# Performance work log

Measured on AMD Instinct MI355X. Metric: run time of the kernel, lower is better.

## Reference

```python
import jax, jax.numpy as jnp
import numpy as np

C = 256; HEADS = 8; LEVELS = 4; POINTS = 4; D = C // HEADS
SPATIAL = np.array([[96, 96], [48, 48], [24, 24], [12, 12]], dtype=np.int32)  # (H, W) per level
AREAS = SPATIAL[:, 0] * SPATIAL[:, 1]
HW = int(AREAS.sum())  # 12240
LSI = np.concatenate([[0], np.cumsum(AREAS)[:-1]]).astype(np.int32)
N = 1; Q = HW


def setup_inputs() -> dict:
    key = jax.random.key(0)
    ks = jax.random.split(key, 12)
    s = 0.02
    return {
        "query": jax.random.normal(ks[0], (N, Q, C), jnp.float32),
        "reference_points": jax.random.uniform(ks[1], (N, Q, LEVELS, 2), jnp.float32),
        "input_flatten": jax.random.normal(ks[2], (N, HW, C), jnp.float32),
        "input_spatial_shapes": jnp.asarray(SPATIAL),
        "input_level_start_index": jnp.asarray(LSI),
        "W_off": jax.random.normal(ks[3], (C, HEADS * LEVELS * POINTS * 2), jnp.float32) * s,
        "b_off": jax.random.normal(ks[4], (HEADS * LEVELS * POINTS * 2,), jnp.float32) * s,
        "W_attn": jax.random.normal(ks[5], (C, HEADS * LEVELS * POINTS), jnp.float32) * s,
        "b_attn": jax.random.normal(ks[6], (HEADS * LEVELS * POINTS,), jnp.float32) * s,
        "W_val": jax.random.normal(ks[7], (C, C), jnp.float32) * (1.0 / np.sqrt(C)),
        "b_val": jax.random.normal(ks[8], (C,), jnp.float32) * s,
        "W_out": jax.random.normal(ks[9], (C, C), jnp.float32) * (1.0 / np.sqrt(C)),
        "b_out": jax.random.normal(ks[10], (C,), jnp.float32) * s,
    }


def _ms_deform_attn(query, reference_points, input_flatten, sp, lsi,
                    W_off, b_off, W_attn, b_attn, W_val, b_val, W_out, b_out):
    n, q, c = query.shape
    hw = input_flatten.shape[1]
    # value projection -> [N, Hd, HW, D]
    value = (input_flatten @ W_val + b_val).reshape(n, hw, HEADS, D).transpose(0, 2, 1, 3)
    # sampling offsets [N,Q,Hd,L,P,2]
    off = (query @ W_off + b_off).reshape(n, q, HEADS, LEVELS, POINTS, 2)
    # attention weights softmaxed over L*P (done inside the fused CUDA kernel)
    attn = jax.nn.softmax((query @ W_attn + b_attn).reshape(n, q, HEADS, LEVELS * POINTS), axis=-1)
    attn = attn.reshape(n, q, HEADS, LEVELS, POINTS)
    # normalized sampling locations (reference_points last dim == 2 branch)
    norm = jnp.stack([sp[:, 1], sp[:, 0]], -1).astype(query.dtype)  # (W, H) per level
    loc = reference_points[:, :, None, :, None, :] + off / norm[None, None, None, :, None, :]
    Hl = sp[:, 0][None, None, None, :, None]
    Wl = sp[:, 1][None, None, None, :, None]
    start = lsi[None, None, None, :, None]
    # grid_sample-style (align_corners=False) pixel coordinates
    x = loc[..., 0] * Wl - 0.5
    y = loc[..., 1] * Hl - 0.5
    x0 = jnp.floor(x); y0 = jnp.floor(y)
    lx = x - x0; ly = y - y0
    x0i = x0.astype(jnp.int32); y0i = y0.astype(jnp.int32)

    def gather(yi, xi):
        valid = (xi >= 0) & (xi < Wl) & (yi >= 0) & (yi < Hl)
        idx = jnp.where(valid, start + yi * Wl + xi, 0)  # [N,Q,Hd,L,P]
        idx_t = idx.transpose(0, 2, 1, 3, 4).reshape(n, HEADS, q * LEVELS * POINTS, 1)
        g = jnp.take_along_axis(value, idx_t, axis=2)  # [N,Hd,Q*L*P,D]
        g = g.reshape(n, HEADS, q, LEVELS, POINTS, D)
        return g * valid.transpose(0, 2, 1, 3, 4)[..., None]

    def w(a):
        return a.transpose(0, 2, 1, 3, 4)[..., None]  # [N,Hd,Q,L,P,1]

    sampled = (gather(y0i, x0i) * w((1 - ly) * (1 - lx))
               + gather(y0i, x0i + 1) * w((1 - ly) * lx)
               + gather(y0i + 1, x0i) * w(ly * (1 - lx))
               + gather(y0i + 1, x0i + 1) * w(ly * lx))  # [N,Hd,Q,L,P,D]
    out = jnp.einsum('nhqlpd,nqhlp->nqhd', sampled, attn).reshape(n, q, c)
    return out @ W_out + b_out


def reference(query, reference_points, input_flatten, input_spatial_shapes, input_level_start_index,
              W_off, b_off, W_attn, b_attn, W_val, b_val, W_out, b_out):
    return _ms_deform_attn(query, reference_points, input_flatten,
                           input_spatial_shapes, input_level_start_index,
                           W_off, b_off, W_attn, b_attn, W_val, b_val, W_out, b_out)
```

## Files before the change

kernel.cpp:

```cpp
#include <hip/hip_runtime.h>

#define QTOT 12240
#define KD   256

typedef float f32x4 __attribute__((ext_vector_type(4)));
typedef short s16x8 __attribute__((ext_vector_type(8)));
typedef short s16x4 __attribute__((ext_vector_type(4)));
typedef unsigned short ushort_t;

__device__ __forceinline__ unsigned short f2b(float x) {
    union { float f; unsigned u; } c; c.f = x;
    unsigned r = c.u + 0x7fffu + ((c.u >> 16) & 1u);
    return (unsigned short)(r >> 16);
}
__device__ __forceinline__ int swz(int row, int kb) { return row * 512 + (kb ^ ((row & 7) << 4)); }

__global__ __launch_bounds__(256) void prep(
    const float* __restrict__ W_val, const float* __restrict__ W_off,
    const float* __restrict__ W_attn, const float* __restrict__ W_out,
    const float* __restrict__ b_off, const float* __restrict__ b_attn,
    ushort_t* __restrict__ WvT, ushort_t* __restrict__ WcT,
    ushort_t* __restrict__ WoT, float* __restrict__ bcomb)
{
    int id = blockIdx.x * 256 + threadIdx.x;
    if (id < 65536) { int n = id >> 8, k = id & 255; WvT[id] = f2b(W_val[k * 256 + n]); }
    else if (id < 163840) {
        int t = id - 65536; int n = t >> 8, k = t & 255;
        float v = (n < 256) ? W_off[k * 256 + n] : W_attn[k * 128 + (n - 256)];
        WcT[t] = f2b(v);
    } else if (id < 229376) {
        int t = id - 163840; int n = t >> 8, k = t & 255;
        WoT[t] = f2b(W_out[k * 256 + n]);
    } else if (id < 229760) {
        int t = id - 229376; bcomb[t] = (t < 256) ? b_off[t] : b_attn[t - 256];
    }
}

__global__ __launch_bounds__(256) void gemm1(
    const float* __restrict__ inflat, const float* __restrict__ query,
    const ushort_t* __restrict__ WvT, const ushort_t* __restrict__ WcT,
    const float* __restrict__ b_val, const float* __restrict__ bcomb,
    ushort_t* __restrict__ projb, ushort_t* __restrict__ offb,
    float* __restrict__ logitf)
{
    __shared__ char As[16384];
    const int b = blockIdx.x;
    const bool isval = b < 383;
    const int bm = (isval ? b : b - 383) * 32;
    const float* A = isval ? inflat : query;
    const ushort_t* WT = isval ? WvT : WcT;
    const int nc = isval ? 4 : 6;

    const int tid = threadIdx.x, lane = tid & 63, wave = tid >> 6;
    const int lr = lane & 15, g8 = (lane >> 4) * 8;

    {
        const float4* srcb = (const float4*)(A + (size_t)bm * KD);
        const int rem_rows = QTOT - bm;
#pragma unroll
        for (int j = 0; j < 8; ++j) {
            const int f4i = j * 256 + tid;
            const int row = f4i >> 6;
            const int colb = (f4i & 63) * 8;
            float4 f = make_float4(0.f, 0.f, 0.f, 0.f);
            if (row < rem_rows) f = srcb[f4i];
            s16x4 v;
            v[0] = f2b(f.x); v[1] = f2b(f.y); v[2] = f2b(f.z); v[3] = f2b(f.w);
            *(s16x4*)(As + swz(row, colb)) = v;
        }
    }
    __syncthreads();

    const int rg = (lane >> 4) * 4;

    for (int c = 0; c < nc; ++c) {
        const int col = c * 64 + wave * 16 + lr;
        s16x8 bfr[8];
        {
            const ushort_t* bp = WT + (size_t)col * KD + g8;
#pragma unroll
            for (int kc = 0; kc < 8; ++kc) bfr[kc] = *(const s16x8*)(bp + kc * 32);
        }
        f32x4 acc[2];
        acc[0] = (f32x4)0.f; acc[1] = (f32x4)0.f;
#pragma unroll
        for (int kc = 0; kc < 8; ++kc) {
            const int kb = (kc * 32 + g8) * 2;
            s16x8 a0 = *(const s16x8*)(As + swz(lr,      kb));
            s16x8 a1 = *(const s16x8*)(As + swz(16 + lr, kb));
            acc[0] = __builtin_amdgcn_mfma_f32_16x16x32_bf16(a0, bfr[kc], acc[0], 0, 0, 0);
            acc[1] = __builtin_amdgcn_mfma_f32_16x16x32_bf16(a1, bfr[kc], acc[1], 0, 0, 0);
        }
        const float bb = isval ? b_val[col] : bcomb[col];
#pragma unroll
        for (int mf = 0; mf < 2; ++mf)
#pragma unroll
            for (int rr = 0; rr < 4; ++rr) {
                const int row = bm + mf * 16 + rg + rr;
                if (row >= QTOT) continue;
                const float v = acc[mf][rr] + bb;
                if (isval)          projb[(size_t)row * 256 + col] = f2b(v);
                else if (col < 256) offb [(size_t)row * 256 + col] = f2b(v);
                else                logitf[(size_t)row * 128 + col - 256] = v;
            }
    }
}

__global__ __launch_bounds__(256) void sample5(
    const float* __restrict__ rp, const ushort_t* __restrict__ offb,
    const float* __restrict__ logitf, const ushort_t* __restrict__ projb,
    const int* __restrict__ sp, const int* __restrict__ lsi,
    ushort_t* __restrict__ outpre)
{
    const int q0 = blockIdx.x * 4;
    const int tid = threadIdx.x;

    __shared__ int   s_idx[512][4];
    __shared__ float s_w[512][4];

#pragma unroll
    for (int rep = 0; rep < 2; ++rep) {
        const int task = rep * 256 + tid;
        const int ql = task >> 7, t = task & 127;
        const int l = (t >> 2) & 3;
        const int q = q0 + ql;

        float logit = logitf[(size_t)q * 128 + t];
        float mx = logit;
#pragma unroll
        for (int d = 1; d < 16; d <<= 1) mx = fmaxf(mx, __shfl_xor(mx, d));
        float e = __expf(logit - mx);
        float s = e;
#pragma unroll
        for (int d = 1; d < 16; d <<= 1) s += __shfl_xor(s, d);
        const float aw = e / s;

        const unsigned opk = *(const unsigned*)&offb[(size_t)q * 256 + t * 2];
        const float ox = __uint_as_float(opk << 16);
        const float oy = __uint_as_float(opk & 0xffff0000u);

        const int Hl = sp[l * 2], Wl = sp[l * 2 + 1], st = lsi[l];
        const float rx = rp[((size_t)q * 4 + l) * 2 + 0];
        const float ry = rp[((size_t)q * 4 + l) * 2 + 1];

        const float x = rx * (float)Wl + ox - 0.5f;
        const float y = ry * (float)Hl + oy - 0.5f;
        const float xf = floorf(x), yf = floorf(y);
        const int x0 = (int)xf, y0 = (int)yf;
        const float lx = x - xf, ly = y - yf;

        const bool vx0 = (x0 >= 0) && (x0 < Wl);
        const bool vx1 = (x0 + 1 >= 0) && (x0 + 1 < Wl);
        const bool vy0 = (y0 >= 0) && (y0 < Hl);
        const bool vy1 = (y0 + 1 >= 0) && (y0 + 1 < Hl);

        s_w[task][0] = (vx0 && vy0) ? aw * (1.f - ly) * (1.f - lx) : 0.f;
        s_w[task][1] = (vx1 && vy0) ? aw * (1.f - ly) * lx         : 0.f;
        s_w[task][2] = (vx0 && vy1) ? aw * ly * (1.f - lx)         : 0.f;
        s_w[task][3] = (vx1 && vy1) ? aw * ly * lx                 : 0.f;
        s_idx[task][0] = (vx0 && vy0) ? (st + y0 * Wl + x0) * 512           : 0;
        s_idx[task][1] = (vx1 && vy0) ? (st + y0 * Wl + x0 + 1) * 512       : 0;
        s_idx[task][2] = (vx0 && vy1) ? (st + (y0 + 1) * Wl + x0) * 512     : 0;
        s_idx[task][3] = (vx1 && vy1) ? (st + (y0 + 1) * Wl + x0 + 1) * 512 : 0;
    }
    __syncthreads();

    const int t = tid & 127, qlA = tid >> 7;
    const int h = t >> 4, pq = (t >> 2) & 3, c8 = t & 3;
    const char* basec = (const char*)projb + (h * 32 + c8 * 8) * 2;

    float aA[8] = {0,0,0,0,0,0,0,0};
    float aB[8] = {0,0,0,0,0,0,0,0};
#pragma unroll
    for (int l = 0; l < 4; ++l) {
        const int slotA = (qlA << 7)       + h * 16 + l * 4 + pq;
        const int slotB = ((qlA + 2) << 7) + h * 16 + l * 4 + pq;
        const int4   iA = *(const int4*)s_idx[slotA];
        const float4 wA = *(const float4*)s_w[slotA];
        const int4   iB = *(const int4*)s_idx[slotB];
        const float4 wB = *(const float4*)s_w[slotB];
#pragma unroll
        for (int c = 0; c < 4; ++c) {
            const int   idA = (c == 0) ? iA.x : (c == 1) ? iA.y : (c == 2) ? iA.z : iA.w;
            const float wwA = (c == 0) ? wA.x : (c == 1) ? wA.y : (c == 2) ? wA.z : wA.w;
            const uint4 v = *(const uint4*)(basec + idA);
            aA[0] += wwA * __uint_as_float(v.x << 16);
            aA[1] += wwA * __uint_as_float(v.x & 0xffff0000u);
            aA[2] += wwA * __uint_as_float(v.y << 16);
            aA[3] += wwA * __uint_as_float(v.y & 0xffff0000u);
            aA[4] += wwA * __uint_as_float(v.z << 16);
            aA[5] += wwA * __uint_as_float(v.z & 0xffff0000u);
            aA[6] += wwA * __uint_as_float(v.w << 16);
            aA[7] += wwA * __uint_as_float(v.w & 0xffff0000u);
        }
#pragma unroll
        for (int c = 0; c < 4; ++c) {
            const int   idB = (c == 0) ? iB.x : (c == 1) ? iB.y : (c == 2) ? iB.z : iB.w;
            const float wwB = (c == 0) ? wB.x : (c == 1) ? wB.y : (c == 2) ? wB.z : wB.w;
            const uint4 v = *(const uint4*)(basec + idB);
            aB[0] += wwB * __uint_as_float(v.x << 16);
            aB[1] += wwB * __uint_as_float(v.x & 0xffff0000u);
            aB[2] += wwB * __uint_as_float(v.y << 16);
            aB[3] += wwB * __uint_as_float(v.y & 0xffff0000u);
            aB[4] += wwB * __uint_as_float(v.z << 16);
            aB[5] += wwB * __uint_as_float(v.z & 0xffff0000u);
            aB[6] += wwB * __uint_as_float(v.w << 16);
            aB[7] += wwB * __uint_as_float(v.w & 0xffff0000u);
        }
    }
#pragma unroll
    for (int i = 0; i < 8; ++i) {
        aA[i] += __shfl_xor(aA[i], 4);  aA[i] += __shfl_xor(aA[i], 8);
        aB[i] += __shfl_xor(aB[i], 4);  aB[i] += __shfl_xor(aB[i], 8);
    }
    if (pq == 0) {
        const int colo = h * 32 + c8 * 8;
        uint4 o;
        o.x = (unsigned)f2b(aA[0]) | ((unsigned)f2b(aA[1]) << 16);
        o.y = (unsigned)f2b(aA[2]) | ((unsigned)f2b(aA[3]) << 16);
        o.z = (unsigned)f2b(aA[4]) | ((unsigned)f2b(aA[5]) << 16);
        o.w = (unsigned)f2b(aA[6]) | ((unsigned)f2b(aA[7]) << 16);
        *(uint4*)&outpre[(size_t)(q0 + qlA) * 256 + colo] = o;
        o.x = (unsigned)f2b(aB[0]) | ((unsigned)f2b(aB[1]) << 16);
        o.y = (unsigned)f2b(aB[2]) | ((unsigned)f2b(aB[3]) << 16);
        o.z = (unsigned)f2b(aB[4]) | ((unsigned)f2b(aB[5]) << 16);
        o.w = (unsigned)f2b(aB[6]) | ((unsigned)f2b(aB[7]) << 16);
        *(uint4*)&outpre[(size_t)(q0 + qlA + 2) * 256 + colo] = o;
    }
}

__global__ __launch_bounds__(256) void gemm_o(
    const ushort_t* __restrict__ Ab, const ushort_t* __restrict__ WoT,
    const float* __restrict__ b_out, float* __restrict__ out)
{
    const int bm = blockIdx.x * 32;
    const int tid = threadIdx.x, lane = tid & 63, wave = tid >> 6;
    const int lr = lane & 15, g8 = (lane >> 4) * 8;
    const int rg = (lane >> 4) * 4;

    const ushort_t* ap0;
    const ushort_t* ap1;
    {
        int r0 = bm + lr;      if (r0 >= QTOT) r0 = QTOT - 1;
        int r1 = bm + 16 + lr; if (r1 >= QTOT) r1 = QTOT - 1;
        ap0 = Ab + (size_t)r0 * KD + g8;
        ap1 = Ab + (size_t)r1 * KD + g8;
    }

#pragma unroll
    for (int c = 0; c < 4; ++c) {
        const int col = c * 64 + wave * 16 + lr;
        s16x8 bfr[8];
        {
            const ushort_t* bp = WoT + (size_t)col * KD + g8;
#pragma unroll
            for (int kc = 0; kc < 8; ++kc) bfr[kc] = *(const s16x8*)(bp + kc * 32);
        }
        f32x4 acc[2];
        acc[0] = (f32x4)0.f; acc[1] = (f32x4)0.f;
#pragma unroll
        for (int kc = 0; kc < 8; ++kc) {
            s16x8 a0 = *(const s16x8*)(ap0 + kc * 32);
            s16x8 a1 = *(const s16x8*)(ap1 + kc * 32);
            acc[0] = __builtin_amdgcn_mfma_f32_16x16x32_bf16(a0, bfr[kc], acc[0], 0, 0, 0);
            acc[1] = __builtin_amdgcn_mfma_f32_16x16x32_bf16(a1, bfr[kc], acc[1], 0, 0, 0);
        }
        const float bb = b_out[col];
#pragma unroll
        for (int mf = 0; mf < 2; ++mf)
#pragma unroll
            for (int rr = 0; rr < 4; ++rr) {
                const int row = bm + mf * 16 + rg + rr;
                if (row < QTOT) out[(size_t)row * 256 + col] = acc[mf][rr] + bb;
            }
    }
}

extern "C" void kernel_launch(void* const* d_in, const int* in_sizes, int n_in,
                              void* d_out, int out_size, void* d_ws, size_t ws_size,
                              hipStream_t stream) {
    const float* query  = (const float*)d_in[0];
    const float* rp     = (const float*)d_in[1];
    const float* inflat = (const float*)d_in[2];
    const int*   sp     = (const int*)d_in[3];
    const int*   lsi    = (const int*)d_in[4];
    const float* W_off  = (const float*)d_in[5];
    const float* b_off  = (const float*)d_in[6];
    const float* W_attn = (const float*)d_in[7];
    const float* b_attn = (const float*)d_in[8];
    const float* W_val  = (const float*)d_in[9];
    const float* b_val  = (const float*)d_in[10];
    const float* W_out  = (const float*)d_in[11];
    const float* b_out  = (const float*)d_in[12];
    float* out = (float*)d_out;

    char* ws = (char*)d_ws;
    ushort_t* projb  = (ushort_t*)ws; ws += (size_t)QTOT * 256 * 2;
    ushort_t* offb   = (ushort_t*)ws; ws += (size_t)QTOT * 256 * 2;
    float*    logitf = (float*)ws;    ws += (size_t)QTOT * 128 * 4;
    ushort_t* outpre = (ushort_t*)ws; ws += (size_t)QTOT * 256 * 2;
    ushort_t* WvT    = (ushort_t*)ws; ws += 65536 * 2;
    ushort_t* WcT    = (ushort_t*)ws; ws += 98304 * 2;
    ushort_t* WoT    = (ushort_t*)ws; ws += 65536 * 2;
    float*    bcomb  = (float*)ws;    ws += 384 * 4;

    prep<<<dim3(898), dim3(256), 0, stream>>>(W_val, W_off, W_attn, W_out, b_off, b_attn,
                                              WvT, WcT, WoT, bcomb);

    gemm1<<<dim3(766), dim3(256), 0, stream>>>(inflat, query, WvT, WcT, b_val, bcomb,
                                               projb, offb, logitf);

    sample5<<<dim3(3060), dim3(256), 0, stream>>>(rp, offb, logitf, projb, sp, lsi, outpre);

    gemm_o<<<dim3(383), dim3(256), 0, stream>>>(outpre, WoT, b_out, out);
}
```

Before: 69.72 us.

## Tile-transpose weight prep, double-buffer B fragments, store logits as bf16, retile output GEMM

Weight prep now transposes each 32x32 tile through shared memory with coalesced float4 reads and vector stores, replacing strided scalar gathers. Both GEMM kernels now prefetch the next column chunk's B fragments while running MFMA on the current chunk. Attention logits are stored as bf16 instead of fp32, halving that intermediate's traffic at some precision cost in the softmax inputs. The output GEMM uses 16-row tiles, giving twice as many blocks, and keeps its A fragments in registers.

```diff
diff --git a/kernel.cpp b/kernel.cpp
--- a/kernel.cpp
+++ b/kernel.cpp
@@ -13,26 +13,92 @@
     unsigned r = c.u + 0x7fffu + ((c.u >> 16) & 1u);
     return (unsigned short)(r >> 16);
 }
+__device__ __forceinline__ float b2f(unsigned short u) {
+    return __uint_as_float((unsigned)u << 16);
+}
 __device__ __forceinline__ int swz(int row, int kb) { return row * 512 + (kb ^ ((row & 7) << 4)); }
 
-__global__ __launch_bounds__(256) void prep(
+__global__ __launch_bounds__(256) void prep2(
     const float* __restrict__ W_val, const float* __restrict__ W_off,
     const float* __restrict__ W_attn, const float* __restrict__ W_out,
     const float* __restrict__ b_off, const float* __restrict__ b_attn,
     ushort_t* __restrict__ WvT, ushort_t* __restrict__ WcT,
     ushort_t* __restrict__ WoT, float* __restrict__ bcomb)
 {
-    int id = blockIdx.x * 256 + threadIdx.x;
-    if (id < 65536) { int n = id >> 8, k = id & 255; WvT[id] = f2b(W_val[k * 256 + n]); }
-    else if (id < 163840) {
-        int t = id - 65536; int n = t >> 8, k = t & 255;
-        float v = (n < 256) ? W_off[k * 256 + n] : W_attn[k * 128 + (n - 256)];
-        WcT[t] = f2b(v);
-    } else if (id < 229376) {
-        int t = id - 163840; int n = t >> 8, k = t & 255;
-        WoT[t] = f2b(W_out[k * 256 + n]);
-    } else if (id < 229760) {
-        int t = id - 229376; bcomb[t] = (t < 256) ? b_off[t] : b_attn[t - 256];
+    const int b = blockIdx.x;
+    if (b == 224) {
+        for (int t = threadIdx.x; t < 384; t += 256)
+            bcomb[t] = (t < 256) ? b_off[t] : b_attn[t - 256];
+        return;
+    }
+    __shared__ ushort_t tile[32][33];
+    const float* src; ushort_t* dst; int kt, nt, srcld, n_off;
+    if (b < 64)       { src = W_val; dst = WvT; kt = b >> 3;        nt = b & 7;        srcld = 256; n_off = 0; }
+    else if (b < 160) { int t = b - 64; dst = WcT; kt = t / 12;     nt = t % 12;
+                        if (nt < 8) { src = W_off;  srcld = 256; n_off = 0; }
+                        else        { src = W_attn; srcld = 128; n_off = 256; } }
+    else              { int t = b - 160; src = W_out; dst = WoT; kt = t >> 3; nt = t & 7; srcld = 256; n_off = 0; }
+
+    {
+        const int r = threadIdx.x >> 3, c4 = (threadIdx.x & 7) * 4;
+        const int gk = kt * 32 + r;
+        const int gs = nt * 32 + c4 - n_off;
+        float4 f = *(const float4*)(src + (size_t)gk * srcld + gs);
+        tile[r][c4 + 0] = f2b(f.x); tile[r][c4 + 1] = f2b(f.y);
+        tile[r][c4 + 2] = f2b(f.z); tile[r][c4 + 3] = f2b(f.w);
+    }
+    __syncthreads();
+    {
+        const int r2 = threadIdx.x >> 3, k4 = (threadIdx.x & 7) * 4;
+        s16x4 v;
+        v[0] = tile[k4 + 0][r2]; v[1] = tile[k4 + 1][r2];
+        v[2] = tile[k4 + 2][r2]; v[3] = tile[k4 + 3][r2];
+        *(s16x4*)(dst + (size_t)(nt * 32 + r2) * 256 + kt * 32 + k4) = v;
+    }
+}
+
+__device__ __forceinline__ void loadB(const ushort_t* __restrict__ WT, int c, s16x8 (&dst)[8]) {
+    const int lane = threadIdx.x & 63, wave = threadIdx.x >> 6;
+    const int lr = lane & 15, g8 = (lane >> 4) * 8;
+    const ushort_t* bp = WT + (size_t)(c * 64 + wave * 16 + lr) * KD + g8;
+#pragma unroll
+    for (int kc = 0; kc < 8; ++kc) dst[kc] = *(const s16x8*)(bp + kc * 32);
+}
+
+template<int MODE>
+__device__ __forceinline__ void g1step(
+    int c, bool pre, const char* As, const ushort_t* __restrict__ WT,
+    const float* __restrict__ bias, ushort_t* __restrict__ o_bf,
+    ushort_t* __restrict__ o_lg, int bm, s16x8 (&cur)[8], s16x8 (&nxt)[8])
+{
+    const int lane = threadIdx.x & 63, wave = threadIdx.x >> 6;
+    const int lr = lane & 15, g8 = (lane >> 4) * 8, rg = (lane >> 4) * 4;
+    if (pre) loadB(WT, c + 1, nxt);
+    f32x4 acc0 = (f32x4)0.f, acc1 = (f32x4)0.f;
+#pragma unroll
+    for (int kc = 0; kc < 8; ++kc) {
+        const int kb = (kc * 32 + g8) * 2;
+        s16x8 a0 = *(const s16x8*)(As + swz(lr,      kb));
+        s16x8 a1 = *(const s16x8*)(As + swz(16 + lr, kb));
+        acc0 = __builtin_amdgcn_mfma_f32_16x16x32_bf16(a0, cur[kc], acc0, 0, 0, 0);
+        acc1 = __builtin_amdgcn_mfma_f32_16x16x32_bf16(a1, cur[kc], acc1, 0, 0, 0);
+    }
+    const int col = c * 64 + wave * 16 + lr;
+    const float bv = bias[col];
+#pragma unroll
+    for (int mf = 0; mf < 2; ++mf) {
+        const f32x4& a = mf ? acc1 : acc0;
+#pragma unroll
+        for (int rr = 0; rr < 4; ++rr) {
+            const int row = bm + mf * 16 + rg + rr;
+            if (row >= QTOT) continue;
+            const float v = a[rr] + bv;
+            if (MODE == 0) o_bf[(size_t)row * 256 + col] = f2b(v);
+            else {
+                if (col < 256) o_bf[(size_t)row * 256 + col] = f2b(v);
+                else           o_lg[(size_t)row * 128 + col - 256] = f2b(v);
+            }
+        }
     }
 }
 
@@ -41,7 +107,7 @@
     const ushort_t* __restrict__ WvT, const ushort_t* __restrict__ WcT,
     const float* __restrict__ b_val, const float* __restrict__ bcomb,
     ushort_t* __restrict__ projb, ushort_t* __restrict__ offb,
-    float* __restrict__ logitf)
+    ushort_t* __restrict__ logitb)
 {
     __shared__ char As[16384];
     const int b = blockIdx.x;
@@ -49,10 +115,10 @@
     const int bm = (isval ? b : b - 383) * 32;
     const float* A = isval ? inflat : query;
     const ushort_t* WT = isval ? WvT : WcT;
-    const int nc = isval ? 4 : 6;
-
-    const int tid = threadIdx.x, lane = tid & 63, wave = tid >> 6;
-    const int lr = lane & 15, g8 = (lane >> 4) * 8;
+    const int tid = threadIdx.x;
+
+    s16x8 b0[8], b1[8];
+    loadB(WT, 0, b0);
 
     {
         const float4* srcb = (const float4*)(A + (size_t)bm * KD);
@@ -71,44 +137,24 @@
     }
     __syncthreads();
 
-    const int rg = (lane >> 4) * 4;
-
-    for (int c = 0; c < nc; ++c) {
-        const int col = c * 64 + wave * 16 + lr;
-        s16x8 bfr[8];
-        {
-            const ushort_t* bp = WT + (size_t)col * KD + g8;
-#pragma unroll
-            for (int kc = 0; kc < 8; ++kc) bfr[kc] = *(const s16x8*)(bp + kc * 32);
-        }
-        f32x4 acc[2];
-        acc[0] = (f32x4)0.f; acc[1] = (f32x4)0.f;
-#pragma unroll
-        for (int kc = 0; kc < 8; ++kc) {
-            const int kb = (kc * 32 + g8) * 2;
-            s16x8 a0 = *(const s16x8*)(As + swz(lr,      kb));
-            s16x8 a1 = *(const s16x8*)(As + swz(16 + lr, kb));
-            acc[0] = __builtin_amdgcn_mfma_f32_16x16x32_bf16(a0, bfr[kc], acc[0], 0, 0, 0);
-            acc[1] = __builtin_amdgcn_mfma_f32_16x16x32_bf16(a1, bfr[kc], acc[1], 0, 0, 0);
-        }
-        const float bb = isval ? b_val[col] : bcomb[col];
-#pragma unroll
-        for (int mf = 0; mf < 2; ++mf)
-#pragma unroll
-            for (int rr = 0; rr < 4; ++rr) {
-                const int row = bm + mf * 16 + rg + rr;
-                if (row >= QTOT) continue;
-                const float v = acc[mf][rr] + bb;
-                if (isval)          projb[(size_t)row * 256 + col] = f2b(v);
-                else if (col < 256) offb [(size_t)row * 256 + col] = f2b(v);
-                else                logitf[(size_t)row * 128 + col - 256] = v;
-            }
+    if (isval) {
+        g1step<0>(0, true,  As, WT, b_val, projb, nullptr, bm, b0, b1);
+        g1step<0>(1, true,  As, WT, b_val, projb, nullptr, bm, b1, b0);
+        g1step<0>(2, true,  As, WT, b_val, projb, nullptr, bm, b0, b1);
+        g1step<0>(3, false, As, WT, b_val, projb, nullptr, bm, b1, b0);
+    } else {
+        g1step<1>(0, true,  As, WT, bcomb, offb, logitb, bm, b0, b1);
+        g1step<1>(1, true,  As, WT, bcomb, offb, logitb, bm, b1, b0);
+        g1step<1>(2, true,  As, WT, bcomb, offb, logitb, bm, b0, b1);
+        g1step<1>(3, true,  As, WT, bcomb, offb, logitb, bm, b1, b0);
+        g1step<1>(4, true,  As, WT, bcomb, offb, logitb, bm, b0, b1);
+        g1step<1>(5, false, As, WT, bcomb, offb, logitb, bm, b1, b0);
     }
 }
 
 __global__ __launch_bounds__(256) void sample5(
     const float* __restrict__ rp, const ushort_t* __restrict__ offb,
-    const float* __restrict__ logitf, const ushort_t* __restrict__ projb,
+    const ushort_t* __restrict__ logitb, const ushort_t* __restrict__ projb,
     const int* __restrict__ sp, const int* __restrict__ lsi,
     ushort_t* __restrict__ outpre)
 {
@@ -125,7 +171,7 @@
         const int l = (t >> 2) & 3;
         const int q = q0 + ql;
 
-        float logit = logitf[(size_t)q * 128 + t];
+        float logit = b2f(logitb[(size_t)q * 128 + t]);
         float mx = logit;
 #pragma unroll
         for (int d = 1; d < 16; d <<= 1) mx = fmaxf(mx, __shfl_xor(mx, d));
@@ -229,50 +275,52 @@
     }
 }
 
-__global__ __launch_bounds__(256) void gemm_o(
+__global__ __launch_bounds__(256) void gemm_o2(
     const ushort_t* __restrict__ Ab, const ushort_t* __restrict__ WoT,
     const float* __restrict__ b_out, float* __restrict__ out)
 {
-    const int bm = blockIdx.x * 32;
-    const int tid = threadIdx.x, lane = tid & 63, wave = tid >> 6;
-    const int lr = lane & 15, g8 = (lane >> 4) * 8;
-    const int rg = (lane >> 4) * 4;
-
-    const ushort_t* ap0;
-    const ushort_t* ap1;
+    const int bm = blockIdx.x * 16;
+    const int lane = threadIdx.x & 63, wave = threadIdx.x >> 6;
+    const int lr = lane & 15, g8 = (lane >> 4) * 8, rg = (lane >> 4) * 4;
+
+    s16x8 b0[8], b1[8];
+    loadB(WoT, 0, b0);
+
+    s16x8 af[8];
     {
-        int r0 = bm + lr;      if (r0 >= QTOT) r0 = QTOT - 1;
-        int r1 = bm + 16 + lr; if (r1 >= QTOT) r1 = QTOT - 1;
-        ap0 = Ab + (size_t)r0 * KD + g8;
-        ap1 = Ab + (size_t)r1 * KD + g8;
-    }
-
-#pragma unroll
-    for (int c = 0; c < 4; ++c) {
-        const int col = c * 64 + wave * 16 + lr;
-        s16x8 bfr[8];
+        const ushort_t* ap = Ab + (size_t)(bm + lr) * KD + g8;
+#pragma unroll
+        for (int kc = 0; kc < 8; ++kc) af[kc] = *(const s16x8*)(ap + kc * 32);
+    }
+
+#pragma unroll
+    for (int cc = 0; cc < 2; ++cc) {
         {
-            const ushort_t* bp = WoT + (size_t)col * KD + g8;
-#pragma unroll
-            for (int kc = 0; kc < 8; ++kc) bfr[kc] = *(const s16x8*)(bp + kc * 32);
-        }
-        f32x4 acc[2];
-        acc[0] = (f32x4)0.f; acc[1] = (f32x4)0.f;
-#pragma unroll
-        for (int kc = 0; kc < 8; ++kc) {
-            s16x8 a0 = *(const s16x8*)(ap0 + kc * 32);
-            s16x8 a1 = *(const s16x8*)(ap1 + kc * 32);
-            acc[0] = __builtin_amdgcn_mfma_f32_16x16x32_bf16(a0, bfr[kc], acc[0], 0, 0, 0);
-            acc[1] = __builtin_amdgcn_mfma_f32_16x16x32_bf16(a1, bfr[kc], acc[1], 0, 0, 0);
-        }
-        const float bb = b_out[col];
-#pragma unroll
-        for (int mf = 0; mf < 2; ++mf)
-#pragma unroll
-            for (int rr = 0; rr < 4; ++rr) {
-                const int row = bm + mf * 16 + rg + rr;
-                if (row < QTOT) out[(size_t)row * 256 + col] = acc[mf][rr] + bb;
-            }
+            const int c = 2 * cc;
+            loadB(WoT, c + 1, b1);
+            f32x4 acc = (f32x4)0.f;
+#pragma unroll
+            for (int kc = 0; kc < 8; ++kc)
+                acc = __builtin_amdgcn_mfma_f32_16x16x32_bf16(af[kc], b0[kc], acc, 0, 0, 0);
+            const int col = c * 64 + wave * 16 + lr;
+            const float bv = b_out[col];
+#pragma unroll
+            for (int rr = 0; rr < 4; ++rr)
+                out[(size_t)(bm + rg + rr) * 256 + col] = acc[rr] + bv;
+        }
+        {
+            const int c = 2 * cc + 1;
+            if (c + 1 < 4) loadB(WoT, c + 1, b0);
+            f32x4 acc = (f32x4)0.f;
+#pragma unroll
+            for (int kc = 0; kc < 8; ++kc)
+                acc = __builtin_amdgcn_mfma_f32_16x16x32_bf16(af[kc], b1[kc], acc, 0, 0, 0);
+            const int col = c * 64 + wave * 16 + lr;
+            const float bv = b_out[col];
+#pragma unroll
+            for (int rr = 0; rr < 4; ++rr)
+                out[(size_t)(bm + rg + rr) * 256 + col] = acc[rr] + bv;
+        }
     }
 }
 
@@ -297,20 +345,20 @@
     char* ws = (char*)d_ws;
     ushort_t* projb  = (ushort_t*)ws; ws += (size_t)QTOT * 256 * 2;
     ushort_t* offb   = (ushort_t*)ws; ws += (size_t)QTOT * 256 * 2;
-    float*    logitf = (float*)ws;    ws += (size_t)QTOT * 128 * 4;
+    ushort_t* logitb = (ushort_t*)ws; ws += (size_t)QTOT * 128 * 2;
     ushort_t* outpre = (ushort_t*)ws; ws += (size_t)QTOT * 256 * 2;
     ushort_t* WvT    = (ushort_t*)ws; ws += 65536 * 2;
     ushort_t* WcT    = (ushort_t*)ws; ws += 98304 * 2;
     ushort_t* WoT    = (ushort_t*)ws; ws += 65536 * 2;
     float*    bcomb  = (float*)ws;    ws += 384 * 4;
 
-    prep<<<dim3(898), dim3(256), 0, stream>>>(W_val, W_off, W_attn, W_out, b_off, b_attn,
-                                              WvT, WcT, WoT, bcomb);
+    prep2<<<dim3(225), dim3(256), 0, stream>>>(W_val, W_off, W_attn, W_out, b_off, b_attn,
+                                               WvT, WcT, WoT, bcomb);
 
     gemm1<<<dim3(766), dim3(256), 0, stream>>>(inflat, query, WvT, WcT, b_val, bcomb,
-                                               projb, offb, logitf);
-
-    sample5<<<dim3(3060), dim3(256), 0, stream>>>(rp, offb, logitf, projb, sp, lsi, outpre);
-
-    gemm_o<<<dim3(383), dim3(256), 0, stream>>>(outpre, WoT, b_out, out);
-}
+                                               projb, offb, logitb);
+
+    sample5<<<dim3(3060), dim3(256), 0, stream>>>(rp, offb, logitb, projb, sp, lsi, outpre);
+
+    gemm_o2<<<dim3(765), dim3(256), 0, stream>>>(outpre, WoT, b_out, out);
+}
```

Result: slower. 82.31 us (+18.1%).
